# Kernel optimization log

Measured on AMD Instinct MI355X. Metric: run time of the kernel, lower is better.

The kernel has to match this reference:

```python
import jax, jax.numpy as jnp
import numpy as np

DIM = 512
HEADS = 8
WIN = 64
HIDDEN = 2048
EPS = 1e-5


def layernorm(x, g, b):
    mu = jnp.mean(x, axis=-1, keepdims=True)
    var = jnp.var(x, axis=-1, keepdims=True)
    return (x - mu) * jax.lax.rsqrt(var + EPS) * g + b


def setup_inputs() -> dict:
    key = jax.random.key(0)
    ks = jax.random.split(key, 10)
    s = lambda fan_in: 1.0 / np.sqrt(fan_in)
    return {
        "x": jax.random.normal(ks[0], (8, 4096, DIM), dtype=jnp.float32),
        "ln1_g": jnp.ones((DIM,), jnp.float32),
        "ln1_b": jnp.zeros((DIM,), jnp.float32),
        "qkv_w": jax.random.normal(ks[1], (DIM, 3 * DIM), jnp.float32) * s(DIM),
        "qkv_b": jnp.zeros((3 * DIM,), jnp.float32),
        "proj_w": jax.random.normal(ks[2], (DIM, DIM), jnp.float32) * s(DIM),
        "proj_b": jnp.zeros((DIM,), jnp.float32),
        "ln2_g": jnp.ones((DIM,), jnp.float32),
        "ln2_b": jnp.zeros((DIM,), jnp.float32),
        "fc1_w": jax.random.normal(ks[3], (DIM, HIDDEN), jnp.float32) * s(DIM),
        "fc1_b": jnp.zeros((HIDDEN,), jnp.float32),
        "fc2_w": jax.random.normal(ks[4], (HIDDEN, DIM), jnp.float32) * s(HIDDEN),
        "fc2_b": jnp.zeros((DIM,), jnp.float32),
    }


def reference(x, ln1_g, ln1_b, qkv_w, qkv_b, proj_w, proj_b, ln2_g, ln2_b,
              fc1_w, fc1_b, fc2_w, fc2_b):
    B, N, C = x.shape
    hd = C // HEADS
    scale = hd ** -0.5

    # --- W-MSA (shift_size forced to 0, attn_mask None) ---
    h = layernorm(x, ln1_g, ln1_b)
    hw = h.reshape(B * (N // WIN), WIN, C)
    qkv = hw @ qkv_w + qkv_b
    qkv = qkv.reshape(-1, WIN, 3, HEADS, hd)
    q = qkv[:, :, 0] * scale
    k = qkv[:, :, 1]
    v = qkv[:, :, 2]
    attn = jnp.einsum('bqhd,bkhd->bhqk', q, k)
    attn = jax.nn.softmax(attn, axis=-1)
    o = jnp.einsum('bhqk,bkhd->bqhd', attn, v).reshape(-1, WIN, C)
    o = o @ proj_w + proj_b
    x = x + o.reshape(B, N, C)

    # --- MLP (GELU exact, dropout=0) ---
    h2 = layernorm(x, ln2_g, ln2_b)
    h2 = jax.nn.gelu(h2 @ fc1_w + fc1_b, approximate=False)
    x = x + (h2 @ fc2_w + fc2_b)
    return x
```

## Files before the change

kernel.cpp:

```cpp
#include <hip/hip_runtime.h>
#include <hip/hip_bf16.h>
#include <cstdint>

typedef unsigned short U16;
typedef float f32x4 __attribute__((ext_vector_type(4)));
typedef __bf16 bf16x8 __attribute__((ext_vector_type(8)));

#define DEVINL __device__ __forceinline__

DEVINL U16 f2bf(float f) {
    unsigned u = __float_as_uint(f);
    return (U16)((u + 0x7FFFu + ((u >> 16) & 1u)) >> 16);
}
DEVINL float bf2f(U16 s) { return __uint_as_float(((unsigned)s) << 16); }

DEVINL void gld16(const void* g, void* l) {
    __builtin_amdgcn_global_load_lds(
        (const __attribute__((address_space(1))) void*)g,
        (__attribute__((address_space(3))) void*)l, 16, 0, 0);
}

#define MFMA_BF16 __builtin_amdgcn_mfma_f32_16x16x32_bf16

__global__ __launch_bounds__(256) void tcast_kernel(const float* __restrict__ w,
                                                    U16* __restrict__ wt, int K, int N) {
    __shared__ float tile[32][33];
    int n0 = blockIdx.x * 32, k0 = blockIdx.y * 32;
    int tx = threadIdx.x, ty = threadIdx.y;
#pragma unroll
    for (int i = 0; i < 32; i += 8) tile[ty + i][tx] = w[(size_t)(k0 + ty + i) * N + (n0 + tx)];
    __syncthreads();
#pragma unroll
    for (int i = 0; i < 32; i += 8) wt[(size_t)(n0 + ty + i) * K + (k0 + tx)] = f2bf(tile[tx][ty + i]);
}

__global__ __launch_bounds__(256) void ln_kernel(const float* __restrict__ x,
                                                 const float* __restrict__ g,
                                                 const float* __restrict__ b,
                                                 U16* __restrict__ out) {
    int lane = threadIdx.x & 63;
    size_t row = (size_t)blockIdx.x * 4 + (threadIdx.x >> 6);
    const float4* xr = (const float4*)(x + row * 512);
    float4 v0 = xr[lane], v1 = xr[lane + 64];
    float s = (v0.x + v0.y) + (v0.z + v0.w) + (v1.x + v1.y) + (v1.z + v1.w);
    float sq = (v0.x * v0.x + v0.y * v0.y + v0.z * v0.z + v0.w * v0.w) +
               (v1.x * v1.x + v1.y * v1.y + v1.z * v1.z + v1.w * v1.w);
#pragma unroll
    for (int m = 1; m < 64; m <<= 1) { s += __shfl_xor(s, m); sq += __shfl_xor(sq, m); }
    float mu = s * (1.f / 512.f);
    float var = sq * (1.f / 512.f) - mu * mu;
    float rs = rsqrtf(var + 1e-5f);
    const float4* g4 = (const float4*)g;
    const float4* b4 = (const float4*)b;
    float4 gv = g4[lane], bv = b4[lane];
    ushort4 o;
    o.x = f2bf((v0.x - mu) * rs * gv.x + bv.x);
    o.y = f2bf((v0.y - mu) * rs * gv.y + bv.y);
    o.z = f2bf((v0.z - mu) * rs * gv.z + bv.z);
    o.w = f2bf((v0.w - mu) * rs * gv.w + bv.w);
    ((ushort4*)(out + row * 512))[lane] = o;
    gv = g4[lane + 64]; bv = b4[lane + 64];
    o.x = f2bf((v1.x - mu) * rs * gv.x + bv.x);
    o.y = f2bf((v1.y - mu) * rs * gv.y + bv.y);
    o.z = f2bf((v1.z - mu) * rs * gv.z + bv.z);
    o.w = f2bf((v1.w - mu) * rs * gv.w + bv.w);
    ((ushort4*)(out + row * 512))[lane + 64] = o;
}

template <int EPI>
__global__ __launch_bounds__(512, 2) void gemm256(const U16* __restrict__ A,
                                                  const U16* __restrict__ Bt,
                                                  const float* __restrict__ bias,
                                                  const float* __restrict__ resid,
                                                  U16* __restrict__ outb,
                                                  float* __restrict__ outf,
                                                  int M, int N, int K, int gridN) {
    __shared__ __align__(16) U16 smem[65536];

    const int tid = threadIdx.x;
    const int lane = tid & 63, wv = tid >> 6;
    const int lo = lane & 15, hi = lane >> 4;
    const int wm = wv >> 2, wn = wv & 3;

    const int nwg = gridDim.x, bid = blockIdx.x;
    const int swz = (bid & 7) * (nwg >> 3) + (bid >> 3);
    const int bn = swz % gridN, bm = swz / gridN;

    const int sr = tid >> 2;
    const int lc = (tid & 3) ^ (sr & 3);
    const U16* gA0 = A + (size_t)(bm * 256 + sr) * K + lc * 8;
    const U16* gB0 = Bt + (size_t)(bn * 256 + sr) * K + lc * 8;

#define STAGE(t2)                                                     \
    do {                                                              \
        const int _b = ((t2) & 3) * 16384;                            \
        const U16* _ga = gA0 + (size_t)(t2) * 32;                     \
        const U16* _gb = gB0 + (size_t)(t2) * 32;                     \
        U16* _la = smem + _b + tid * 8;                               \
        U16* _lb = smem + _b + 8192 + tid * 8;                        \
        gld16(_ga, _la);                                              \
        gld16(_ga + (size_t)128 * K, _la + 4096);                     \
        gld16(_gb, _lb);                                              \
        gld16(_gb + (size_t)128 * K, _lb + 4096);                     \
    } while (0)

    const int ck = (hi ^ (lo & 3)) << 3;

    f32x4 acc[8][4] = {};

    const int nt = K >> 5;
    STAGE(0);
    STAGE(1);

    for (int t = 0; t < nt; ++t) {
        if (t + 2 < nt) {
            STAGE(t + 2);
            asm volatile("s_waitcnt vmcnt(8)" ::: "memory");
        } else if (t + 1 < nt) {
            asm volatile("s_waitcnt vmcnt(4)" ::: "memory");
        } else {
            asm volatile("s_waitcnt vmcnt(0)" ::: "memory");
        }
        asm volatile("s_barrier" ::: "memory");

        const int cb = (t & 3) * 16384;
        const U16* Abuf = smem + cb + wm * 4096;
        const U16* Bbuf = smem + cb + 8192 + (wn >> 1) * 4096;
        const int brow = (wn & 1) * 64;

        bf16x8 af[8], bg[4];
#pragma unroll
        for (int j = 0; j < 4; ++j)
            bg[j] = *(const bf16x8*)(Bbuf + (brow + j * 16 + lo) * 32 + ck);
#pragma unroll
        for (int i = 0; i < 8; ++i)
            af[i] = *(const bf16x8*)(Abuf + (i * 16 + lo) * 32 + ck);

        __builtin_amdgcn_s_setprio(1);
#pragma unroll
        for (int i = 0; i < 8; ++i)
#pragma unroll
            for (int j = 0; j < 4; ++j)
                acc[i][j] = MFMA_BF16(af[i], bg[j], acc[i][j], 0, 0, 0);
        __builtin_amdgcn_s_setprio(0);
    }

    const int row0 = bm * 256 + wm * 128 + hi * 4;
    const int col0 = bn * 256 + wn * 64 + lo;
    float bc[4];
#pragma unroll
    for (int j = 0; j < 4; ++j) bc[j] = bias[col0 + j * 16];

    if (EPI == 1) {
#pragma unroll
        for (int i = 0; i < 8; ++i)
#pragma unroll
            for (int r = 0; r < 4; ++r) {
                const size_t rowb = (size_t)(row0 + i * 16 + r) * N;
#pragma unroll
                for (int j = 0; j < 4; ++j) {
                    const size_t idx = rowb + col0 + j * 16;
                    outf[idx] = acc[i][j][r] + bc[j] + resid[idx];
                }
            }
    } else {
#pragma unroll
        for (int i = 0; i < 8; ++i)
#pragma unroll
            for (int j = 0; j < 4; ++j)
#pragma unroll
                for (int r = 0; r < 4; ++r) {
                    float v = acc[i][j][r] + bc[j];
                    if (EPI == 2) v = 0.5f * v * (1.f + erff(v * 0.70710678118654752f));
                    outb[(size_t)(row0 + i * 16 + r) * N + col0 + j * 16] = f2bf(v);
                }
    }
#undef STAGE
}

__global__ __launch_bounds__(256) void attn_kernel(const U16* __restrict__ qkv,
                                                   U16* __restrict__ o) {
    const int blk = blockIdx.x;
    const int w = blk >> 3, h = blk & 7;
    const int tid = threadIdx.x;
    const int lane = tid & 63, wv = tid >> 6;
    const int lo = lane & 15, hi = lane >> 4;

    __shared__ __align__(16) U16 Qs[64][72];
    __shared__ __align__(16) U16 Ks[64][72];
    __shared__ __align__(16) U16 Vt[64][72];
    __shared__ __align__(16) U16 Ps[4][16][72];

    {
        const int r = tid >> 2;
        const int c0 = (tid & 3) << 4;
        const U16* p = qkv + (size_t)(w * 64 + r) * 1536 + h * 64 + c0;
        *(bf16x8*)&Ks[r][c0] = *(const bf16x8*)(p + 512);
        *(bf16x8*)&Ks[r][c0 + 8] = *(const bf16x8*)(p + 520);
        const U16* pv = p + 1024;
#pragma unroll
        for (int i = 0; i < 16; i++) Vt[c0 + i][r] = pv[i];
#pragma unroll
        for (int i = 0; i < 16; i++) Qs[r][c0 + i] = f2bf(bf2f(p[i]) * 0.125f);
    }
    __syncthreads();

    const int rb = wv * 16;
    f32x4 s[4] = {};
#pragma unroll
    for (int dc = 0; dc < 64; dc += 32) {
        bf16x8 a = *(const bf16x8*)&Qs[rb + lo][dc + hi * 8];
#pragma unroll
        for (int jb = 0; jb < 4; jb++) {
            bf16x8 bfr = *(const bf16x8*)&Ks[jb * 16 + lo][dc + hi * 8];
            s[jb] = MFMA_BF16(a, bfr, s[jb], 0, 0, 0);
        }
    }
#pragma unroll
    for (int r = 0; r < 4; r++) {
        float m = fmaxf(fmaxf(s[0][r], s[1][r]), fmaxf(s[2][r], s[3][r]));
#pragma unroll
        for (int msk = 1; msk < 16; msk <<= 1) m = fmaxf(m, __shfl_xor(m, msk));
        float e[4], sum = 0.f;
#pragma unroll
        for (int jb = 0; jb < 4; jb++) { e[jb] = expf(s[jb][r] - m); sum += e[jb]; }
#pragma unroll
        for (int msk = 1; msk < 16; msk <<= 1) sum += __shfl_xor(sum, msk);
        float inv = 1.f / sum;
#pragma unroll
        for (int jb = 0; jb < 4; jb++) Ps[wv][hi * 4 + r][jb * 16 + lo] = f2bf(e[jb] * inv);
    }
    __syncthreads();

    f32x4 oa[4] = {};
#pragma unroll
    for (int jc = 0; jc < 64; jc += 32) {
        bf16x8 a = *(const bf16x8*)&Ps[wv][lo][jc + hi * 8];
#pragma unroll
        for (int db = 0; db < 4; db++) {
            bf16x8 bfr = *(const bf16x8*)&Vt[db * 16 + lo][jc + hi * 8];
            oa[db] = MFMA_BF16(a, bfr, oa[db], 0, 0, 0);
        }
    }
#pragma unroll
    for (int db = 0; db < 4; db++)
#pragma unroll
        for (int r = 0; r < 4; r++)
            o[(size_t)(w * 64 + rb + hi * 4 + r) * 512 + h * 64 + db * 16 + lo] = f2bf(oa[db][r]);
}

extern "C" void kernel_launch(void* const* d_in, const int* in_sizes, int n_in,
                              void* d_out, int out_size, void* d_ws, size_t ws_size,
                              hipStream_t stream) {
    const float* x = (const float*)d_in[0];
    const float* ln1_g = (const float*)d_in[1];
    const float* ln1_b = (const float*)d_in[2];
    const float* qkv_w = (const float*)d_in[3];
    const float* qkv_b = (const float*)d_in[4];
    const float* proj_w = (const float*)d_in[5];
    const float* proj_b = (const float*)d_in[6];
    const float* ln2_g = (const float*)d_in[7];
    const float* ln2_b = (const float*)d_in[8];
    const float* fc1_w = (const float*)d_in[9];
    const float* fc1_b = (const float*)d_in[10];
    const float* fc2_w = (const float*)d_in[11];
    const float* fc2_b = (const float*)d_in[12];
    float* out = (float*)d_out;

    char* ws = (char*)d_ws;
    U16* hbuf = (U16*)ws;
    U16* big = (U16*)(ws + 33554432);
    U16* wt_qkv = (U16*)(ws + 33554432 + 134217728);
    U16* wt_proj = wt_qkv + 1536 * 512;
    U16* wt_fc1 = wt_proj + 512 * 512;
    U16* wt_fc2 = wt_fc1 + 2048 * 512;

    dim3 tb(32, 8);
    tcast_kernel<<<dim3(1536 / 32, 512 / 32), tb, 0, stream>>>(qkv_w, wt_qkv, 512, 1536);
    tcast_kernel<<<dim3(512 / 32, 512 / 32), tb, 0, stream>>>(proj_w, wt_proj, 512, 512);
    tcast_kernel<<<dim3(2048 / 32, 512 / 32), tb, 0, stream>>>(fc1_w, wt_fc1, 512, 2048);
    tcast_kernel<<<dim3(512 / 32, 2048 / 32), tb, 0, stream>>>(fc2_w, wt_fc2, 2048, 512);

    ln_kernel<<<8192, 256, 0, stream>>>(x, ln1_g, ln1_b, hbuf);
    gemm256<0><<<768, 512, 0, stream>>>(hbuf, wt_qkv, qkv_b, nullptr, big, nullptr, 32768, 1536, 512, 6);
    attn_kernel<<<4096, 256, 0, stream>>>(big, hbuf);
    gemm256<1><<<256, 512, 0, stream>>>(hbuf, wt_proj, proj_b, x, nullptr, out, 32768, 512, 512, 2);
    ln_kernel<<<8192, 256, 0, stream>>>(out, ln2_g, ln2_b, hbuf);
    gemm256<2><<<1024, 512, 0, stream>>>(hbuf, wt_fc1, fc1_b, nullptr, big, nullptr, 32768, 2048, 512, 8);
    gemm256<1><<<256, 512, 0, stream>>>(big, wt_fc2, fc2_b, out, nullptr, out, 32768, 512, 2048, 2);
}
```

Measured before the change: 413.5 us.

## Shrink GEMM tile to 128x256 with triple-buffered LDS and higher occupancy

The GEMM kernel goes from 256x256 to 128x256 output tiles per workgroup. The LDS pipeline drops from four stage buffers to three, and the next stage is issued after the barrier. The launch bound asks for 4 workgroups per CU and the grids double, which is meant to improve occupancy and load balance, especially for the N=512 GEMMs that previously launched only 256 blocks. The trade-off is less data reuse per tile, more global traffic for B, and a changed LDS swizzle pattern.

After: 389.0 us. 5.9% less time.

```diff
diff --git a/kernel.cpp b/kernel.cpp
--- a/kernel.cpp
+++ b/kernel.cpp
@@ -68,14 +68,14 @@
 }
 
 template <int EPI>
-__global__ __launch_bounds__(512, 2) void gemm256(const U16* __restrict__ A,
+__global__ __launch_bounds__(512, 4) void gemm_rt(const U16* __restrict__ A,
                                                   const U16* __restrict__ Bt,
                                                   const float* __restrict__ bias,
                                                   const float* __restrict__ resid,
                                                   U16* __restrict__ outb,
                                                   float* __restrict__ outf,
                                                   int M, int N, int K, int gridN) {
-    __shared__ __align__(16) U16 smem[65536];
+    __shared__ __align__(16) U16 smem[36864];
 
     const int tid = threadIdx.x;
     const int lane = tid & 63, wv = tid >> 6;
@@ -83,69 +83,61 @@
     const int wm = wv >> 2, wn = wv & 3;
 
     const int nwg = gridDim.x, bid = blockIdx.x;
-    const int swz = (bid & 7) * (nwg >> 3) + (bid >> 3);
-    const int bn = swz % gridN, bm = swz / gridN;
+    const int swzb = (bid & 7) * (nwg >> 3) + (bid >> 3);
+    const int bn = swzb % gridN, bm = swzb / gridN;
 
     const int sr = tid >> 2;
-    const int lc = (tid & 3) ^ (sr & 3);
-    const U16* gA0 = A + (size_t)(bm * 256 + sr) * K + lc * 8;
+    const int lc = (tid & 3) ^ ((sr >> 2) & 3);
+    const U16* gA0 = A + (size_t)(bm * 128 + sr) * K + lc * 8;
     const U16* gB0 = Bt + (size_t)(bn * 256 + sr) * K + lc * 8;
 
 #define STAGE(t2)                                                     \
     do {                                                              \
-        const int _b = ((t2) & 3) * 16384;                            \
+        U16* _l = smem + ((t2) % 3) * 12288 + tid * 8;                \
         const U16* _ga = gA0 + (size_t)(t2) * 32;                     \
         const U16* _gb = gB0 + (size_t)(t2) * 32;                     \
-        U16* _la = smem + _b + tid * 8;                               \
-        U16* _lb = smem + _b + 8192 + tid * 8;                        \
-        gld16(_ga, _la);                                              \
-        gld16(_ga + (size_t)128 * K, _la + 4096);                     \
-        gld16(_gb, _lb);                                              \
-        gld16(_gb + (size_t)128 * K, _lb + 4096);                     \
+        gld16(_ga, _l);                                               \
+        gld16(_gb, _l + 4096);                                        \
+        gld16(_gb + (size_t)128 * K, _l + 8192);                      \
     } while (0)
 
-    const int ck = (hi ^ (lo & 3)) << 3;
-
-    f32x4 acc[8][4] = {};
+    const int ck = (hi ^ ((lo >> 2) & 3)) << 3;
+
+    f32x4 acc[4][4] = {};
 
     const int nt = K >> 5;
     STAGE(0);
     STAGE(1);
 
     for (int t = 0; t < nt; ++t) {
-        if (t + 2 < nt) {
-            STAGE(t + 2);
-            asm volatile("s_waitcnt vmcnt(8)" ::: "memory");
-        } else if (t + 1 < nt) {
-            asm volatile("s_waitcnt vmcnt(4)" ::: "memory");
+        if (t + 1 < nt) {
+            asm volatile("s_waitcnt vmcnt(3)" ::: "memory");
         } else {
             asm volatile("s_waitcnt vmcnt(0)" ::: "memory");
         }
-        asm volatile("s_barrier" ::: "memory");
-
-        const int cb = (t & 3) * 16384;
-        const U16* Abuf = smem + cb + wm * 4096;
-        const U16* Bbuf = smem + cb + 8192 + (wn >> 1) * 4096;
-        const int brow = (wn & 1) * 64;
-
-        bf16x8 af[8], bg[4];
-#pragma unroll
-        for (int j = 0; j < 4; ++j)
-            bg[j] = *(const bf16x8*)(Bbuf + (brow + j * 16 + lo) * 32 + ck);
-#pragma unroll
-        for (int i = 0; i < 8; ++i)
-            af[i] = *(const bf16x8*)(Abuf + (i * 16 + lo) * 32 + ck);
+        __builtin_amdgcn_s_barrier();
+        if (t + 2 < nt) STAGE(t + 2);
+
+        const int cb = (t % 3) * 12288;
+        const U16* Ab = smem + cb + (wm * 64 + lo) * 32 + ck;
+        const U16* Bb = smem + cb + 4096 + (wn >> 1) * 4096 + ((wn & 1) * 64 + lo) * 32 + ck;
+
+        bf16x8 af[4], bg[4];
+#pragma unroll
+        for (int i = 0; i < 4; ++i) af[i] = *(const bf16x8*)(Ab + i * 512);
+#pragma unroll
+        for (int j = 0; j < 4; ++j) bg[j] = *(const bf16x8*)(Bb + j * 512);
 
         __builtin_amdgcn_s_setprio(1);
 #pragma unroll
-        for (int i = 0; i < 8; ++i)
+        for (int i = 0; i < 4; ++i)
 #pragma unroll
             for (int j = 0; j < 4; ++j)
                 acc[i][j] = MFMA_BF16(af[i], bg[j], acc[i][j], 0, 0, 0);
         __builtin_amdgcn_s_setprio(0);
     }
 
-    const int row0 = bm * 256 + wm * 128 + hi * 4;
+    const int row0 = bm * 128 + wm * 64 + hi * 4;
     const int col0 = bn * 256 + wn * 64 + lo;
     float bc[4];
 #pragma unroll
@@ -153,7 +145,7 @@
 
     if (EPI == 1) {
 #pragma unroll
-        for (int i = 0; i < 8; ++i)
+        for (int i = 0; i < 4; ++i)
 #pragma unroll
             for (int r = 0; r < 4; ++r) {
                 const size_t rowb = (size_t)(row0 + i * 16 + r) * N;
@@ -165,7 +157,7 @@
             }
     } else {
 #pragma unroll
-        for (int i = 0; i < 8; ++i)
+        for (int i = 0; i < 4; ++i)
 #pragma unroll
             for (int j = 0; j < 4; ++j)
 #pragma unroll
@@ -282,10 +274,10 @@
     tcast_kernel<<<dim3(512 / 32, 2048 / 32), tb, 0, stream>>>(fc2_w, wt_fc2, 2048, 512);
 
     ln_kernel<<<8192, 256, 0, stream>>>(x, ln1_g, ln1_b, hbuf);
-    gemm256<0><<<768, 512, 0, stream>>>(hbuf, wt_qkv, qkv_b, nullptr, big, nullptr, 32768, 1536, 512, 6);
+    gemm_rt<0><<<1536, 512, 0, stream>>>(hbuf, wt_qkv, qkv_b, nullptr, big, nullptr, 32768, 1536, 512, 6);
     attn_kernel<<<4096, 256, 0, stream>>>(big, hbuf);
-    gemm256<1><<<256, 512, 0, stream>>>(hbuf, wt_proj, proj_b, x, nullptr, out, 32768, 512, 512, 2);
+    gemm_rt<1><<<512, 512, 0, stream>>>(hbuf, wt_proj, proj_b, x, nullptr, out, 32768, 512, 512, 2);
     ln_kernel<<<8192, 256, 0, stream>>>(out, ln2_g, ln2_b, hbuf);
-    gemm256<2><<<1024, 512, 0, stream>>>(hbuf, wt_fc1, fc1_b, nullptr, big, nullptr, 32768, 2048, 512, 8);
-    gemm256<1><<<256, 512, 0, stream>>>(big, wt_fc2, fc2_b, out, nullptr, out, 32768, 512, 2048, 2);
-}
+    gemm_rt<2><<<2048, 512, 0, stream>>>(hbuf, wt_fc1, fc1_b, nullptr, big, nullptr, 32768, 2048, 512, 8);
+    gemm_rt<1><<<512, 512, 0, stream>>>(big, wt_fc2, fc2_b, out, nullptr, out, 32768, 512, 2048, 2);
+}
```
